# Kernel optimization log

Hardware: AMD Instinct MI355X
Metric: run time of the kernel (lower is better)

## Reference

```python
import jax, jax.numpy as jnp
import numpy as np

B, H, W, C = 16, 64, 64, 512
WS, SS, NH = 8, 4, 16
HD = C // NH
N = WS * WS          # tokens per window = 64
NWH, NWW = H // WS, W // WS
NW = NWH * NWW       # windows per image = 64
HID = 2048
EPS = 1e-5

def _rel_pos_index():
    coords = np.stack(np.meshgrid(np.arange(WS), np.arange(WS), indexing='ij'))  # [2,ws,ws]
    cf = coords.reshape(2, -1)                      # [2,N]
    rel = cf[:, :, None] - cf[:, None, :]           # [2,N,N]
    rel = rel.transpose(1, 2, 0).astype(np.int64)   # [N,N,2]
    rel[:, :, 0] += WS - 1
    rel[:, :, 1] += WS - 1
    rel[:, :, 0] *= 2 * WS - 1
    return rel.sum(-1)                              # [N,N]

def _attn_mask():
    img = np.zeros((H, W), dtype=np.float32)
    cnt = 0
    sls = (slice(0, -WS), slice(-WS, -SS), slice(-SS, None))
    for hs in sls:
        for ws_ in sls:
            img[hs, ws_] = cnt
            cnt += 1
    mw = img.reshape(NWH, WS, NWW, WS).transpose(0, 2, 1, 3).reshape(-1, N)  # [nW,N]
    am = mw[:, None, :] - mw[:, :, None]            # [nW,N,N] (unsqueeze(1)-unsqueeze(2))
    return np.where(am != 0, np.float32(-100.0), np.float32(0.0))

_RPI = jnp.asarray(_rel_pos_index())
_AMASK = jnp.asarray(_attn_mask())

def _ln(x, g, b):
    m = jnp.mean(x, -1, keepdims=True)
    v = jnp.mean((x - m) ** 2, -1, keepdims=True)
    return (x - m) * jax.lax.rsqrt(v + EPS) * g + b

def setup_inputs() -> dict:
    key = jax.random.key(0)
    ks = jax.random.split(key, 8)
    s = 0.02
    return {
        'x': jax.random.normal(ks[0], (B, H * W, C), jnp.float32),
        'g1': jnp.ones((C,), jnp.float32), 'b1': jnp.zeros((C,), jnp.float32),
        'qkv_w': jax.random.normal(ks[1], (C, 3 * C), jnp.float32) * s,
        'qkv_b': jnp.zeros((3 * C,), jnp.float32),
        'proj_w': jax.random.normal(ks[2], (C, C), jnp.float32) * s,
        'proj_b': jnp.zeros((C,), jnp.float32),
        'rpb': jax.random.normal(ks[3], ((2 * WS - 1) ** 2, NH), jnp.float32) * s,
        'g2': jnp.ones((C,), jnp.float32), 'b2': jnp.zeros((C,), jnp.float32),
        'fc1_w': jax.random.normal(ks[4], (C, HID), jnp.float32) * s,
        'fc1_b': jnp.zeros((HID,), jnp.float32),
        'fc2_w': jax.random.normal(ks[5], (HID, C), jnp.float32) * s,
        'fc2_b': jnp.zeros((C,), jnp.float32),
    }

def reference(x, g1, b1, qkv_w, qkv_b, proj_w, proj_b, rpb, g2, b2, fc1_w, fc1_b, fc2_w, fc2_b):
    shortcut = x                                    # [B,L,C]
    xn = _ln(x, g1, b1).reshape(B, H, W, C)
    xs = jnp.roll(xn, (-SS, -SS), axis=(1, 2))      # cyclic shift
    # window partition -> [B*nW, N, C]
    xw = xs.reshape(B, NWH, WS, NWW, WS, C).transpose(0, 1, 3, 2, 4, 5).reshape(-1, N, C)
    # attention
    qkv = xw @ qkv_w + qkv_b                        # [Bw,N,3C]
    qkv = qkv.reshape(-1, N, 3, NH, HD).transpose(2, 0, 3, 1, 4)  # [3,Bw,NH,N,HD]
    q, k, v = qkv[0], qkv[1], qkv[2]
    scale = jnp.asarray(HD ** -0.5, xw.dtype)
    attn = jnp.einsum('bhnd,bhmd->bhnm', q, k) * scale            # [Bw,NH,N,N]
    bias = rpb[_RPI.reshape(-1)].reshape(N, N, NH).transpose(2, 0, 1)
    attn = attn + bias[None]
    attn = attn.reshape(B, NW, NH, N, N) + _AMASK[None, :, None]
    attn = jax.nn.softmax(attn.reshape(-1, NH, N, N), axis=-1)
    out = jnp.einsum('bhnm,bhmd->bhnd', attn, v)    # [Bw,NH,N,HD]
    out = out.transpose(0, 2, 1, 3).reshape(-1, N, C)
    out = out @ proj_w + proj_b
    # window reverse -> [B,H,W,C]
    xr = out.reshape(B, NWH, NWW, WS, WS, C).transpose(0, 1, 3, 2, 4, 5).reshape(B, H, W, C)
    xr = jnp.roll(xr, (SS, SS), axis=(1, 2)).reshape(B, H * W, C)
    x = shortcut + xr
    h = _ln(x, g2, b2)
    h = jax.nn.gelu(h @ fc1_w + fc1_b, approximate=False) @ fc2_w + fc2_b
    return x + h
```

## Files before the change

kernel.cpp:

```cpp
#include <hip/hip_runtime.h>
#include <hip/hip_bf16.h>

using f32x4  = __attribute__((ext_vector_type(4))) float;
using bf16x8 = __attribute__((ext_vector_type(8))) short;
using short8 = __attribute__((ext_vector_type(8))) short;
using s16x4  = __attribute__((ext_vector_type(4))) short;

#define DEVINL __device__ __forceinline__

DEVINL short f2bf(float f) {
  unsigned u = __builtin_bit_cast(unsigned, f);
  u += 0x7fffu + ((u >> 16) & 1u);
  return (short)(u >> 16);
}

DEVINL float gelu_fast(float v) {
  float t = __expf(-1.5957691216057308f * (v + 0.044715f * v * v * v));
  return v * __builtin_amdgcn_rcpf(1.0f + t);
}

#define GLDS16(g, l) __builtin_amdgcn_global_load_lds( \
    (const __attribute__((address_space(1))) void*)(g), \
    (__attribute__((address_space(3))) void*)(l), 16, 0, 0)

#define SBAR() __builtin_amdgcn_s_barrier()
#define WAITV(n) asm volatile("s_waitcnt vmcnt(" #n ")" ::: "memory")

__global__ __launch_bounds__(256)
void transpose_bf16(const float* __restrict__ in, short* __restrict__ out, int R, int C) {
  int idx = blockIdx.x * 256 + threadIdx.x;
  if (idx >= R * C) return;
  int c = idx / R, r = idx % R;
  out[idx] = f2bf(in[(size_t)r * C + c]);
}

__global__ __launch_bounds__(256)
void bias_expand(const float* __restrict__ rpb, float* __restrict__ BIASF) {
  int idx = blockIdx.x * 256 + threadIdx.x;
  int head = idx >> 12, n = (idx >> 6) & 63, m = idx & 63;
  int i1 = n >> 3, j1 = n & 7, i2 = m >> 3, j2 = m & 7;
  BIASF[idx] = rpb[((i1 - i2 + 7) * 15 + (j1 - j2 + 7)) * 16 + head];
}

template<int REMAP>
__global__ __launch_bounds__(256)
void ln_kernel(const float* __restrict__ X, const float* __restrict__ gamma,
               const float* __restrict__ beta, short* __restrict__ OUT) {
  const int lane = threadIdx.x & 63;
  const int wid  = threadIdx.x >> 6;
  const int t    = blockIdx.x * 4 + wid;
  const float* xp = X + (size_t)t * 512 + lane * 8;
  float4 a = *(const float4*)xp;
  float4 b = *(const float4*)(xp + 4);
  float s = a.x + a.y + a.z + a.w + b.x + b.y + b.z + b.w;
  float q = a.x*a.x + a.y*a.y + a.z*a.z + a.w*a.w
          + b.x*b.x + b.y*b.y + b.z*b.z + b.w*b.w;
#pragma unroll
  for (int d = 1; d < 64; d <<= 1) { s += __shfl_xor(s, d); q += __shfl_xor(q, d); }
  float mean = s * (1.0f / 512.0f);
  float var  = q * (1.0f / 512.0f) - mean * mean;
  float rstd = rsqrtf(var + 1e-5f);
  float4 g0 = *(const float4*)(gamma + lane * 8);
  float4 g1 = *(const float4*)(gamma + lane * 8 + 4);
  float4 b0 = *(const float4*)(beta + lane * 8);
  float4 b1 = *(const float4*)(beta + lane * 8 + 4);
  short8 o;
  o[0] = f2bf((a.x - mean) * rstd * g0.x + b0.x);
  o[1] = f2bf((a.y - mean) * rstd * g0.y + b0.y);
  o[2] = f2bf((a.z - mean) * rstd * g0.z + b0.z);
  o[3] = f2bf((a.w - mean) * rstd * g0.w + b0.w);
  o[4] = f2bf((b.x - mean) * rstd * g1.x + b1.x);
  o[5] = f2bf((b.y - mean) * rstd * g1.y + b1.y);
  o[6] = f2bf((b.z - mean) * rstd * g1.z + b1.z);
  o[7] = f2bf((b.w - mean) * rstd * g1.w + b1.w);
  size_t orow;
  if (REMAP) {
    int bb = t >> 12, l = t & 4095, hh = l >> 6, ww = l & 63;
    int hs = (hh + 60) & 63, ws2 = (ww + 60) & 63;
    orow = (size_t)(bb * 64 + (hs >> 3) * 8 + (ws2 >> 3)) * 64 + (hs & 7) * 8 + (ws2 & 7);
  } else {
    orow = (size_t)t;
  }
  *(short8*)(OUT + orow * 512 + lane * 8) = o;
}

__global__ __launch_bounds__(256)
void attn_core(const short* __restrict__ Q, const short* __restrict__ Kb,
               const short* __restrict__ VT, const float* __restrict__ BIASF,
               short* __restrict__ AOUT) {
  __shared__ short P[4][4096];
  const int tid = threadIdx.x, lane = tid & 63, wid = tid >> 6;
  const int lr = lane & 15, lg = lane >> 4;
  const int gw = blockIdx.x * 4 + wid;
  const int win = gw >> 4, head = gw & 15;
  const int wimg = win & 63, wh = wimg >> 3, ww = wimg & 7;
  const size_t qbase = (size_t)win * 64 * 512 + head * 32;
  short* Pb = P[wid];

  bf16x8 aq[4], bk[4];
#pragma unroll
  for (int tm = 0; tm < 4; ++tm) aq[tm] = *(const bf16x8*)(Q  + qbase + (size_t)(tm * 16 + lr) * 512 + lg * 8);
#pragma unroll
  for (int tn = 0; tn < 4; ++tn) bk[tn] = *(const bf16x8*)(Kb + qbase + (size_t)(tn * 16 + lr) * 512 + lg * 8);
  f32x4 sa[4][4] = {};
#pragma unroll
  for (int tm = 0; tm < 4; ++tm)
#pragma unroll
    for (int tn = 0; tn < 4; ++tn)
      sa[tm][tn] = __builtin_amdgcn_mfma_f32_16x16x32_bf16(aq[tm], bk[tn], sa[tm][tn], 0, 0, 0);

  const float* bias_h = BIASF + head * 4096;
  float inv[4][4];
#pragma unroll
  for (int tm = 0; tm < 4; ++tm) {
#pragma unroll
    for (int e = 0; e < 4; ++e) {
      const int n = tm * 16 + lg * 4 + e;
      const int i1 = n >> 3, j1 = n & 7;
      const int rh1 = (wh == 7) ? 1 + (i1 >> 2) : 0;
      const int rw1 = (ww == 7) ? 1 + (j1 >> 2) : 0;
      float v[4];
      float mx = -3.0e38f;
#pragma unroll
      for (int tn = 0; tn < 4; ++tn) {
        const int m = tn * 16 + lr;
        const int mi = (m >> 3), mj = m & 7;
        const int rh2 = (wh == 7) ? 1 + (mi >> 2) : 0;
        const int rw2 = (ww == 7) ? 1 + (mj >> 2) : 0;
        float val = sa[tm][tn][e] + bias_h[n * 64 + m]
                  + ((rh1 != rh2 || rw1 != rw2) ? -100.0f : 0.0f);
        v[tn] = val;
        mx = fmaxf(mx, val);
      }
#pragma unroll
      for (int d = 1; d < 16; d <<= 1) mx = fmaxf(mx, __shfl_xor(mx, d));
      float sum = 0.f;
#pragma unroll
      for (int tn = 0; tn < 4; ++tn) { v[tn] = __expf(v[tn] - mx); sum += v[tn]; }
#pragma unroll
      for (int d = 1; d < 16; d <<= 1) sum += __shfl_xor(sum, d);
      inv[tm][e] = 1.0f / sum;
      const int sw = (n & 7) << 3;
#pragma unroll
      for (int tn = 0; tn < 4; ++tn) Pb[n * 64 + ((tn * 16 + lr) ^ sw)] = f2bf(v[tn]);
    }
  }
  __syncthreads();

  f32x4 oa[4][2] = {};
  const short* vt = VT + (size_t)win * 32768 + head * 2048;
#pragma unroll
  for (int ks = 0; ks < 2; ++ks) {
    bf16x8 pa[4], bv[2];
#pragma unroll
    for (int tm = 0; tm < 4; ++tm) {
      const int r = tm * 16 + lr;
      pa[tm] = *(const bf16x8*)(Pb + r * 64 + ((ks * 32 + lg * 8) ^ ((r & 7) << 3)));
    }
#pragma unroll
    for (int t2 = 0; t2 < 2; ++t2) bv[t2] = *(const bf16x8*)(vt + (t2 * 16 + lr) * 64 + ks * 32 + lg * 8);
#pragma unroll
    for (int tm = 0; tm < 4; ++tm)
#pragma unroll
      for (int t2 = 0; t2 < 2; ++t2)
        oa[tm][t2] = __builtin_amdgcn_mfma_f32_16x16x32_bf16(pa[tm], bv[t2], oa[tm][t2], 0, 0, 0);
  }
#pragma unroll
  for (int tm = 0; tm < 4; ++tm)
#pragma unroll
    for (int t2 = 0; t2 < 2; ++t2)
#pragma unroll
      for (int e = 0; e < 4; ++e) {
        const int n = tm * 16 + lg * 4 + e;
        AOUT[((size_t)win * 64 + n) * 512 + head * 32 + t2 * 16 + lr] = f2bf(oa[tm][t2][e] * inv[tm][e]);
      }
}

template<int EPI, int K>
__global__ __launch_bounds__(512, 1)
void gemm256(const short* __restrict__ Aa, const short* __restrict__ Bb,
             const float* __restrict__ bias, const float* __restrict__ resid,
             float* __restrict__ outf, short* __restrict__ outh) {
  constexpr int NT = K / 32;
  __shared__ short L[2][2][2][128 * 32];
  const int tid = threadIdx.x;
  const int lane = tid & 63, w = tid >> 6;
  const int lr = lane & 15, lg = lane >> 4;
  const int wm = w >> 2, wn = w & 3;

  const int nwg = gridDim.x;
  const int id = blockIdx.x;
  const int id2 = (id & 7) * (nwg >> 3) + (id >> 3);
  int mt, ntile;
  if (EPI == 1)      { mt = id2 & 7;  ntile = id2 >> 3; }
  else if (EPI == 3) { ntile = id2 % 6; mt = id2 / 6; }
  else               { ntile = id2 & 1; mt = id2 >> 1; }
  const int m0 = mt * 256, n0 = ntile * 256;

  const int srow = w * 16 + (lane >> 2);
  const int pcb  = (lane & 3) * 16;
  const int scol = ((lane & 3) * 8) ^ (((srow >> 1) & 3) * 8);
  const short* gA0 = Aa + (size_t)(m0 +       srow) * K + scol;
  const short* gA1 = Aa + (size_t)(m0 + 128 + srow) * K + scol;
  const short* gB0 = Bb + (size_t)(n0 +       srow) * K + scol;
  const short* gB1 = Bb + (size_t)(n0 + 128 + srow) * K + scol;
  const int dOff = srow * 64 + pcb;
  char* Lb = (char*)&L[0][0][0][0];

  auto stageAll = [&](int slot, int kt) {
    char* s = Lb + slot * 32768 + dOff;
    GLDS16(gA0 + kt * 32, s);
    GLDS16(gA1 + kt * 32, s + 8192);
    GLDS16(gB0 + kt * 32, s + 16384);
    GLDS16(gB1 + kt * 32, s + 24576);
  };

  int aoff[8], boff[4];
#pragma unroll
  for (int mr = 0; mr < 8; ++mr) {
    const int row = mr * 16 + lr;
    aoff[mr] = wm * 8192 + row * 64 + ((lg * 16) ^ (((row >> 1) & 3) * 16));
  }
#pragma unroll
  for (int nr = 0; nr < 4; ++nr) {
    const int row = (wn & 1) * 64 + nr * 16 + lr;
    boff[nr] = 16384 + (wn >> 1) * 8192 + row * 64 + ((lg * 16) ^ (((row >> 1) & 3) * 16));
  }

  f32x4 acc[8][4] = {};
  stageAll(0, 0);
  stageAll(1, 1);
  WAITV(4);
  SBAR();

  for (int t = 0; t < NT; ++t) {
    const char* Ls = Lb + (t & 1) * 32768;
    bf16x8 a[8], b[4];
#pragma unroll
    for (int i = 0; i < 8; ++i) a[i] = *(const bf16x8*)(Ls + aoff[i]);
#pragma unroll
    for (int j = 0; j < 4; ++j) b[j] = *(const bf16x8*)(Ls + boff[j]);
    __builtin_amdgcn_s_setprio(1);
#pragma unroll
    for (int i = 0; i < 8; ++i)
#pragma unroll
      for (int j = 0; j < 4; ++j)
        acc[i][j] = __builtin_amdgcn_mfma_f32_16x16x32_bf16(a[i], b[j], acc[i][j], 0, 0, 0);
    __builtin_amdgcn_s_setprio(0);
    SBAR();
    if (t + 2 < NT) { stageAll(t & 1, t + 2); WAITV(4); }
    else            { WAITV(0); }
    SBAR();
  }

  if (EPI == 1) {
#pragma unroll
    for (int mr = 0; mr < 8; ++mr) {
      const int h0 = m0 + wm * 128 + mr * 16 + lg * 4;
      const float4 bi = *(const float4*)(bias + h0);
#pragma unroll
      for (int nr = 0; nr < 4; ++nr) {
        const int tok = n0 + wn * 64 + nr * 16 + lr;
        s16x4 o;
        o[0] = f2bf(gelu_fast(acc[mr][nr][0] + bi.x));
        o[1] = f2bf(gelu_fast(acc[mr][nr][1] + bi.y));
        o[2] = f2bf(gelu_fast(acc[mr][nr][2] + bi.z));
        o[3] = f2bf(gelu_fast(acc[mr][nr][3] + bi.w));
        *(s16x4*)(outh + (size_t)tok * 2048 + h0) = o;
      }
    }
  } else if (EPI == 0) {
#pragma unroll
    for (int nr = 0; nr < 4; ++nr) {
      const int col = n0 + wn * 64 + nr * 16 + lr;
      const float bc = bias[col];
#pragma unroll
      for (int mr = 0; mr < 8; ++mr)
#pragma unroll
        for (int e = 0; e < 4; ++e) {
          const int row = m0 + wm * 128 + mr * 16 + lg * 4 + e;
          float v = acc[mr][nr][e] + bc;
          const int wv = row >> 6, n = row & 63;
          const int bb = wv >> 6, wi = wv & 63;
          const int hs = (wi >> 3) * 8 + (n >> 3), ws2 = (wi & 7) * 8 + (n & 7);
          const int hh = (hs + 4) & 63, wwp = (ws2 + 4) & 63;
          const size_t orow = (size_t)bb * 4096 + hh * 64 + wwp;
          outf[orow * 512 + col] = resid[orow * 512 + col] + v;
        }
    }
  } else if (EPI == 2) {
#pragma unroll
    for (int nr = 0; nr < 4; ++nr) {
      const int col = n0 + wn * 64 + nr * 16 + lr;
      const float bc = bias[col];
#pragma unroll
      for (int mr = 0; mr < 8; ++mr)
#pragma unroll
        for (int e = 0; e < 4; ++e) {
          const int row = m0 + wm * 128 + mr * 16 + lg * 4 + e;
          outf[(size_t)row * 512 + col] = acc[mr][nr][e] + bc + resid[(size_t)row * 512 + col];
        }
    }
  } else {
    const int seg = n0 >> 9;
#pragma unroll
    for (int nr = 0; nr < 4; ++nr) {
      const int col = n0 + wn * 64 + nr * 16 + lr;
      const float bc = bias[col];
#pragma unroll
      for (int mr = 0; mr < 8; ++mr) {
        const int row0 = m0 + wm * 128 + mr * 16 + lg * 4;
        if (seg == 2) {
          const int cc = col - 1024;
          s16x4 o;
#pragma unroll
          for (int e = 0; e < 4; ++e) o[e] = f2bf(acc[mr][nr][e] + bc);
          *(s16x4*)(outh + 67108864 +
                    (size_t)((row0 >> 6) * 16 + (cc >> 5)) * 2048 + (cc & 31) * 64 + (row0 & 63)) = o;
        } else {
#pragma unroll
          for (int e = 0; e < 4; ++e) {
            const int row = row0 + e;
            float v = acc[mr][nr][e] + bc;
            if (seg == 0) outh[(size_t)row * 512 + col] = f2bf(v * 0.17677669529663687f);
            else          outh[33554432 + (size_t)row * 512 + (col - 512)] = f2bf(v);
          }
        }
      }
    }
  }
}

extern "C" void kernel_launch(void* const* d_in, const int* in_sizes, int n_in,
                              void* d_out, int out_size, void* d_ws, size_t ws_size,
                              hipStream_t stream) {
  (void)in_sizes; (void)n_in; (void)out_size; (void)ws_size;
  const float* x      = (const float*)d_in[0];
  const float* g1     = (const float*)d_in[1];
  const float* b1     = (const float*)d_in[2];
  const float* qkv_w  = (const float*)d_in[3];
  const float* qkv_b  = (const float*)d_in[4];
  const float* proj_w = (const float*)d_in[5];
  const float* proj_b = (const float*)d_in[6];
  const float* rpb    = (const float*)d_in[7];
  const float* g2     = (const float*)d_in[8];
  const float* b2     = (const float*)d_in[9];
  const float* fc1_w  = (const float*)d_in[10];
  const float* fc1_b  = (const float*)d_in[11];
  const float* fc2_w  = (const float*)d_in[12];
  const float* fc2_b  = (const float*)d_in[13];
  float* out = (float*)d_out;
  char* ws = (char*)d_ws;

  short* WQKVT  = (short*)(ws);
  short* WPROJT = (short*)(ws + 1572864);
  short* WFC1T  = (short*)(ws + 2097152);
  short* WFC2T  = (short*)(ws + 4194304);
  float* X2     = (float*)(ws + 6291456);
  float* BIASF  = (float*)(ws + 6291456);
  short* ATT    = (short*)(ws + 140509184);
  short* XW     = (short*)(ws + 207618048);
  short* QB     = (short*)(ws + 274726912);
  short* H1     = XW;
  short* X2N    = ATT;

  transpose_bf16<<<3072, 256, 0, stream>>>(qkv_w,  WQKVT, 512, 1536);
  transpose_bf16<<<1024, 256, 0, stream>>>(proj_w, WPROJT, 512, 512);
  transpose_bf16<<<4096, 256, 0, stream>>>(fc1_w,  WFC1T, 512, 2048);
  transpose_bf16<<<4096, 256, 0, stream>>>(fc2_w,  WFC2T, 2048, 512);
  bias_expand<<<256, 256, 0, stream>>>(rpb, BIASF);

  ln_kernel<1><<<16384, 256, 0, stream>>>(x, g1, b1, XW);
  gemm256<3, 512><<<1536, 512, 0, stream>>>(XW, WQKVT, qkv_b, nullptr, nullptr, QB);
  attn_core<<<4096, 256, 0, stream>>>(QB, QB + 33554432, QB + 67108864, BIASF, ATT);
  gemm256<0, 512><<<512, 512, 0, stream>>>(ATT, WPROJT, proj_b, x, X2, nullptr);
  ln_kernel<0><<<16384, 256, 0, stream>>>(X2, g2, b2, X2N);
  gemm256<1, 512><<<2048, 512, 0, stream>>>(WFC1T, X2N, fc1_b, nullptr, nullptr, H1);
  gemm256<2, 2048><<<512, 512, 0, stream>>>(H1, WFC2T, fc2_b, X2, out, nullptr);
}
```

Before: 980.6 us.

## Switch GEMMs to 128x128 tiles with triple-buffered LDS and single barrier

Replaces the 256x256, 512-thread GEMM with a 128x128 tile, 256-thread kernel that uses a three-slot LDS ring. The next stage's loads are issued before the MFMAs, so one barrier per k-step suffices where two were used before. Smaller tiles and a lower register/LDS footprint allow multiple workgroups per CU and more blocks for better load balance. In exchange, each block does less operand reuse, so more global/L2 traffic per FLOP.

Result: faster. 870.1 us (-11.3%).

```diff
diff --git a/kernel.cpp b/kernel.cpp
--- a/kernel.cpp
+++ b/kernel.cpp
@@ -176,110 +176,110 @@
       }
 }
 
-template<int EPI, int K>
-__global__ __launch_bounds__(512, 1)
-void gemm256(const short* __restrict__ Aa, const short* __restrict__ Bb,
-             const float* __restrict__ bias, const float* __restrict__ resid,
-             float* __restrict__ outf, short* __restrict__ outh) {
+template<int EPI, int K, int NX>
+__global__ __launch_bounds__(256)
+void gemm128v2(const short* __restrict__ Aa, const short* __restrict__ Bb,
+               const float* __restrict__ bias, const float* __restrict__ resid,
+               float* __restrict__ outf, short* __restrict__ outh) {
   constexpr int NT = K / 32;
-  __shared__ short L[2][2][2][128 * 32];
+  __shared__ short L[3][2][128 * 32];
   const int tid = threadIdx.x;
-  const int lane = tid & 63, w = tid >> 6;
+  const int lane = tid & 63, wid = tid >> 6;
   const int lr = lane & 15, lg = lane >> 4;
-  const int wm = w >> 2, wn = w & 3;
+  const int wm = wid >> 1, wn = wid & 1;
 
   const int nwg = gridDim.x;
   const int id = blockIdx.x;
   const int id2 = (id & 7) * (nwg >> 3) + (id >> 3);
   int mt, ntile;
-  if (EPI == 1)      { mt = id2 & 7;  ntile = id2 >> 3; }
-  else if (EPI == 3) { ntile = id2 % 6; mt = id2 / 6; }
-  else               { ntile = id2 & 1; mt = id2 >> 1; }
-  const int m0 = mt * 256, n0 = ntile * 256;
-
-  const int srow = w * 16 + (lane >> 2);
-  const int pcb  = (lane & 3) * 16;
-  const int scol = ((lane & 3) * 8) ^ (((srow >> 1) & 3) * 8);
-  const short* gA0 = Aa + (size_t)(m0 +       srow) * K + scol;
-  const short* gA1 = Aa + (size_t)(m0 + 128 + srow) * K + scol;
-  const short* gB0 = Bb + (size_t)(n0 +       srow) * K + scol;
-  const short* gB1 = Bb + (size_t)(n0 + 128 + srow) * K + scol;
-  const int dOff = srow * 64 + pcb;
-  char* Lb = (char*)&L[0][0][0][0];
-
-  auto stageAll = [&](int slot, int kt) {
-    char* s = Lb + slot * 32768 + dOff;
-    GLDS16(gA0 + kt * 32, s);
-    GLDS16(gA1 + kt * 32, s + 8192);
-    GLDS16(gB0 + kt * 32, s + 16384);
-    GLDS16(gB1 + kt * 32, s + 24576);
+  if (EPI == 1) { mt = id2 % NX; ntile = id2 / NX; }
+  else          { ntile = id2 % NX; mt = id2 / NX; }
+  const int m0 = mt * 128, n0 = ntile * 128;
+
+  const int r0 = tid >> 2, r1 = r0 + 64;
+  const int cb = (tid & 3) * 16;
+  const int sc0 = ((tid & 3) * 8) ^ (((r0 >> 1) & 3) * 8);
+  const int sc1 = ((tid & 3) * 8) ^ (((r1 >> 1) & 3) * 8);
+  const short* gA0 = Aa + (size_t)(m0 + r0) * K + sc0;
+  const short* gA1 = Aa + (size_t)(m0 + r1) * K + sc1;
+  const short* gB0 = Bb + (size_t)(n0 + r0) * K + sc0;
+  const short* gB1 = Bb + (size_t)(n0 + r1) * K + sc1;
+  const int d0 = r0 * 64 + cb, d1 = r1 * 64 + cb;
+  char* Lb = (char*)&L[0][0][0];
+
+  auto stage = [&](int slot, int kt) {
+    char* s = Lb + slot * 16384;
+    GLDS16(gA0 + kt * 32, s + d0);
+    GLDS16(gA1 + kt * 32, s + d1);
+    GLDS16(gB0 + kt * 32, s + 8192 + d0);
+    GLDS16(gB1 + kt * 32, s + 8192 + d1);
   };
 
-  int aoff[8], boff[4];
-#pragma unroll
-  for (int mr = 0; mr < 8; ++mr) {
-    const int row = mr * 16 + lr;
-    aoff[mr] = wm * 8192 + row * 64 + ((lg * 16) ^ (((row >> 1) & 3) * 16));
+  int aoff[4], boff[4];
+#pragma unroll
+  for (int mr = 0; mr < 4; ++mr) {
+    const int row = wm * 64 + mr * 16 + lr;
+    aoff[mr] = row * 64 + ((lg * 16) ^ (((row >> 1) & 3) * 16));
   }
 #pragma unroll
   for (int nr = 0; nr < 4; ++nr) {
-    const int row = (wn & 1) * 64 + nr * 16 + lr;
-    boff[nr] = 16384 + (wn >> 1) * 8192 + row * 64 + ((lg * 16) ^ (((row >> 1) & 3) * 16));
-  }
-
-  f32x4 acc[8][4] = {};
-  stageAll(0, 0);
-  stageAll(1, 1);
+    const int row = wn * 64 + nr * 16 + lr;
+    boff[nr] = 8192 + row * 64 + ((lg * 16) ^ (((row >> 1) & 3) * 16));
+  }
+
+  f32x4 acc[4][4] = {};
+  stage(0, 0);
+  stage(1, 1);
   WAITV(4);
   SBAR();
 
   for (int t = 0; t < NT; ++t) {
-    const char* Ls = Lb + (t & 1) * 32768;
-    bf16x8 a[8], b[4];
-#pragma unroll
-    for (int i = 0; i < 8; ++i) a[i] = *(const bf16x8*)(Ls + aoff[i]);
+    const char* Ls = Lb + (t % 3) * 16384;
+    bf16x8 a[4], b[4];
+#pragma unroll
+    for (int i = 0; i < 4; ++i) a[i] = *(const bf16x8*)(Ls + aoff[i]);
 #pragma unroll
     for (int j = 0; j < 4; ++j) b[j] = *(const bf16x8*)(Ls + boff[j]);
+    if (t + 2 < NT) stage((t + 2) % 3, t + 2);
     __builtin_amdgcn_s_setprio(1);
 #pragma unroll
-    for (int i = 0; i < 8; ++i)
+    for (int i = 0; i < 4; ++i)
 #pragma unroll
       for (int j = 0; j < 4; ++j)
         acc[i][j] = __builtin_amdgcn_mfma_f32_16x16x32_bf16(a[i], b[j], acc[i][j], 0, 0, 0);
     __builtin_amdgcn_s_setprio(0);
+    if (t < NT - 2)       { WAITV(4); }
+    else if (t == NT - 2) { WAITV(0); }
     SBAR();
-    if (t + 2 < NT) { stageAll(t & 1, t + 2); WAITV(4); }
-    else            { WAITV(0); }
-    SBAR();
   }
 
   if (EPI == 1) {
 #pragma unroll
-    for (int mr = 0; mr < 8; ++mr) {
-      const int h0 = m0 + wm * 128 + mr * 16 + lg * 4;
+    for (int i = 0; i < 4; ++i) {
+      const int h0 = m0 + wm * 64 + i * 16 + lg * 4;
       const float4 bi = *(const float4*)(bias + h0);
 #pragma unroll
-      for (int nr = 0; nr < 4; ++nr) {
-        const int tok = n0 + wn * 64 + nr * 16 + lr;
+      for (int j = 0; j < 4; ++j) {
+        const int tok = n0 + wn * 64 + j * 16 + lr;
         s16x4 o;
-        o[0] = f2bf(gelu_fast(acc[mr][nr][0] + bi.x));
-        o[1] = f2bf(gelu_fast(acc[mr][nr][1] + bi.y));
-        o[2] = f2bf(gelu_fast(acc[mr][nr][2] + bi.z));
-        o[3] = f2bf(gelu_fast(acc[mr][nr][3] + bi.w));
+        o[0] = f2bf(gelu_fast(acc[i][j][0] + bi.x));
+        o[1] = f2bf(gelu_fast(acc[i][j][1] + bi.y));
+        o[2] = f2bf(gelu_fast(acc[i][j][2] + bi.z));
+        o[3] = f2bf(gelu_fast(acc[i][j][3] + bi.w));
         *(s16x4*)(outh + (size_t)tok * 2048 + h0) = o;
       }
     }
   } else if (EPI == 0) {
 #pragma unroll
-    for (int nr = 0; nr < 4; ++nr) {
-      const int col = n0 + wn * 64 + nr * 16 + lr;
+    for (int j = 0; j < 4; ++j) {
+      const int col = n0 + wn * 64 + j * 16 + lr;
       const float bc = bias[col];
 #pragma unroll
-      for (int mr = 0; mr < 8; ++mr)
+      for (int i = 0; i < 4; ++i)
 #pragma unroll
         for (int e = 0; e < 4; ++e) {
-          const int row = m0 + wm * 128 + mr * 16 + lg * 4 + e;
-          float v = acc[mr][nr][e] + bc;
+          const int row = m0 + wm * 64 + i * 16 + lg * 4 + e;
+          float v = acc[i][j][e] + bc;
           const int wv = row >> 6, n = row & 63;
           const int bb = wv >> 6, wi = wv & 63;
           const int hs = (wi >> 3) * 8 + (n >> 3), ws2 = (wi & 7) * 8 + (n & 7);
@@ -290,38 +290,38 @@
     }
   } else if (EPI == 2) {
 #pragma unroll
-    for (int nr = 0; nr < 4; ++nr) {
-      const int col = n0 + wn * 64 + nr * 16 + lr;
+    for (int j = 0; j < 4; ++j) {
+      const int col = n0 + wn * 64 + j * 16 + lr;
       const float bc = bias[col];
 #pragma unroll
-      for (int mr = 0; mr < 8; ++mr)
+      for (int i = 0; i < 4; ++i)
 #pragma unroll
         for (int e = 0; e < 4; ++e) {
-          const int row = m0 + wm * 128 + mr * 16 + lg * 4 + e;
-          outf[(size_t)row * 512 + col] = acc[mr][nr][e] + bc + resid[(size_t)row * 512 + col];
+          const int row = m0 + wm * 64 + i * 16 + lg * 4 + e;
+          outf[(size_t)row * 512 + col] = acc[i][j][e] + bc + resid[(size_t)row * 512 + col];
         }
     }
   } else {
     const int seg = n0 >> 9;
 #pragma unroll
-    for (int nr = 0; nr < 4; ++nr) {
-      const int col = n0 + wn * 64 + nr * 16 + lr;
+    for (int j = 0; j < 4; ++j) {
+      const int col = n0 + wn * 64 + j * 16 + lr;
       const float bc = bias[col];
 #pragma unroll
-      for (int mr = 0; mr < 8; ++mr) {
-        const int row0 = m0 + wm * 128 + mr * 16 + lg * 4;
+      for (int i = 0; i < 4; ++i) {
+        const int row0 = m0 + wm * 64 + i * 16 + lg * 4;
         if (seg == 2) {
           const int cc = col - 1024;
           s16x4 o;
 #pragma unroll
-          for (int e = 0; e < 4; ++e) o[e] = f2bf(acc[mr][nr][e] + bc);
+          for (int e = 0; e < 4; ++e) o[e] = f2bf(acc[i][j][e] + bc);
           *(s16x4*)(outh + 67108864 +
                     (size_t)((row0 >> 6) * 16 + (cc >> 5)) * 2048 + (cc & 31) * 64 + (row0 & 63)) = o;
         } else {
 #pragma unroll
           for (int e = 0; e < 4; ++e) {
             const int row = row0 + e;
-            float v = acc[mr][nr][e] + bc;
+            float v = acc[i][j][e] + bc;
             if (seg == 0) outh[(size_t)row * 512 + col] = f2bf(v * 0.17677669529663687f);
             else          outh[33554432 + (size_t)row * 512 + (col - 512)] = f2bf(v);
           }
@@ -371,10 +371,10 @@
   bias_expand<<<256, 256, 0, stream>>>(rpb, BIASF);
 
   ln_kernel<1><<<16384, 256, 0, stream>>>(x, g1, b1, XW);
-  gemm256<3, 512><<<1536, 512, 0, stream>>>(XW, WQKVT, qkv_b, nullptr, nullptr, QB);
+  gemm128v2<3, 512, 12><<<6144, 256, 0, stream>>>(XW, WQKVT, qkv_b, nullptr, nullptr, QB);
   attn_core<<<4096, 256, 0, stream>>>(QB, QB + 33554432, QB + 67108864, BIASF, ATT);
-  gemm256<0, 512><<<512, 512, 0, stream>>>(ATT, WPROJT, proj_b, x, X2, nullptr);
+  gemm128v2<0, 512, 4><<<2048, 256, 0, stream>>>(ATT, WPROJT, proj_b, x, X2, nullptr);
   ln_kernel<0><<<16384, 256, 0, stream>>>(X2, g2, b2, X2N);
-  gemm256<1, 512><<<2048, 512, 0, stream>>>(WFC1T, X2N, fc1_b, nullptr, nullptr, H1);
-  gemm256<2, 2048><<<512, 512, 0, stream>>>(H1, WFC2T, fc2_b, X2, out, nullptr);
-}
+  gemm128v2<1, 512, 16><<<8192, 256, 0, stream>>>(WFC1T, X2N, fc1_b, nullptr, nullptr, H1);
+  gemm128v2<2, 2048, 4><<<2048, 256, 0, stream>>>(H1, WFC2T, fc2_b, X2, out, nullptr);
+}
```
